# Kernel optimization log

Measured on AMD Instinct MI355X. Metric: run time of the kernel, lower is better.

## Reference

```python
import jax, jax.numpy as jnp
import numpy as np

B, Q, V, H = 8, 128, 512, 512


def setup_inputs() -> dict:
    key = jax.random.key(0)
    ks = jax.random.split(key, 6)
    s = 1.0 / np.sqrt(H)
    return {
        "query": jax.random.normal(ks[0], (B, Q, H), jnp.float32),
        "values": jax.random.normal(ks[1], (B, V, H), jnp.float32),
        "mask": jax.random.randint(ks[2], (B, V), 0, 2, jnp.int32),
        "Wq": jax.random.normal(ks[3], (H, H), jnp.float32) * s,
        "bq": jnp.zeros((H,), jnp.float32),
        "Wv": jax.random.normal(ks[4], (H, H), jnp.float32) * s,
        "bv": jnp.zeros((H,), jnp.float32),
        "wc": jax.random.normal(ks[5], (H, 1), jnp.float32) * s,
        "bc": jnp.zeros((1,), jnp.float32),
    }


def reference(query, values, mask, Wq, bq, Wv, bv, wc, bc):
    # Project once per token (Q*H and V*H GEMMs), then broadcast-add:
    # faithful to tanh(Lq(q)[:, :, None] + Lv(v)[:, None]) since Linear is
    # applied along the last dim and broadcasting commutes with it.
    qp = jnp.einsum('bqh,kh->bqk', query, Wq) + bq          # [B,Q,H]
    vp = jnp.einsum('bvh,kh->bvk', values, Wv) + bv          # [B,V,H]
    added = jnp.tanh(qp[:, :, None, :] + vp[:, None, :, :])  # [B,Q,V,H]
    scores = jnp.einsum('bqvh,ho->bqv', added, wc) + bc[0]   # [B,Q,V]
    neg_inf = jnp.array(-jnp.inf, scores.dtype)
    scores = jnp.where(mask[:, None, :] == 0, neg_inf, scores)
    weights = jax.nn.softmax(scores, axis=-1)                # [B,Q,V]
    context = jnp.einsum('bqv,bvh->bqh', weights, values)    # [B,Q,H]
    return (context, weights)
```

## Files before the change

kernel.cpp:

```cpp
#include <hip/hip_runtime.h>
#include <hip/hip_bf16.h>


#define C_SCALE 2.8853900817779268f

typedef __attribute__((ext_vector_type(8))) short short8;
typedef __attribute__((ext_vector_type(4))) float f32x4;

__device__ __forceinline__ float fexp2(float x) { return __builtin_amdgcn_exp2f(x); }
__device__ __forceinline__ float frcp(float x)  { return __builtin_amdgcn_rcpf(x); }
__device__ __forceinline__ short f2bf(float x) {
  __hip_bfloat16 h = __float2bfloat16(x);
  return __builtin_bit_cast(short, h);
}
__device__ __forceinline__ float bf2f(short s) {
  return __bfloat162float(__builtin_bit_cast(__hip_bfloat16, s));
}

__global__ __launch_bounds__(256) void proj_gemm_mfma(
    const float* __restrict__ query, const float* __restrict__ values,
    const float* __restrict__ Wq, const float* __restrict__ Wv,
    const float* __restrict__ bq, const float* __restrict__ bv,
    float* __restrict__ qp, float* __restrict__ vp)
{
  __shared__ short sAhi[64 * 72];
  __shared__ short sAlo[64 * 72];
  __shared__ short sWhi[64 * 72];
  __shared__ short sWlo[64 * 72];

  const int t    = threadIdx.x;
  const int lane = t & 63;
  const int w    = t >> 6;
  const int by   = blockIdx.y;
  const bool isQ = (by < 16);
  const float* A    = isQ ? query : values;
  const float* W    = isQ ? Wq : Wv;
  const float* bias = isQ ? bq : bv;
  float*       out  = isQ ? qp : vp;
  const int m0 = (isQ ? by : (by - 16)) << 6;
  const int n0 = blockIdx.x << 6;

  const int srow = t >> 2, scol = t & 3;
  const float* Ap = A + (size_t)(m0 + srow) * 512 + (scol << 2);
  const float* Wp = W + (size_t)(n0 + srow) * 512 + (scol << 2);

  const int mw = (w & 1) << 5, nw = (w >> 1) << 5;
  const int frow = lane & 15, fquad = lane >> 4;

  f32x4 acc[2][2] = {};
  float4 pfA[4], pfW[4];
#pragma unroll
  for (int p = 0; p < 4; ++p) {
    pfA[p] = *(const float4*)(Ap + (p << 4));
    pfW[p] = *(const float4*)(Wp + (p << 4));
  }

  for (int kc = 0; kc < 512; kc += 64) {
    __syncthreads();
#pragma unroll
    for (int p = 0; p < 4; ++p) {
      float av[4] = {pfA[p].x, pfA[p].y, pfA[p].z, pfA[p].w};
      float wv[4] = {pfW[p].x, pfW[p].y, pfW[p].z, pfW[p].w};
      short4 ah, al, wh, wl;
      short* ahp = (short*)&ah; short* alp = (short*)&al;
      short* whp = (short*)&wh; short* wlp = (short*)&wl;
#pragma unroll
      for (int k = 0; k < 4; ++k) {
        short h1 = f2bf(av[k]); ahp[k] = h1; alp[k] = f2bf(av[k] - bf2f(h1));
        short h2 = f2bf(wv[k]); whp[k] = h2; wlp[k] = f2bf(wv[k] - bf2f(h2));
      }
      const int ofs = srow * 72 + ((p << 2) + scol) * 4;
      *(short4*)&sAhi[ofs] = ah; *(short4*)&sAlo[ofs] = al;
      *(short4*)&sWhi[ofs] = wh; *(short4*)&sWlo[ofs] = wl;
    }
    __syncthreads();
    if (kc + 64 < 512) {
#pragma unroll
      for (int p = 0; p < 4; ++p) {
        pfA[p] = *(const float4*)(Ap + kc + 64 + (p << 4));
        pfW[p] = *(const float4*)(Wp + kc + 64 + (p << 4));
      }
    }
#pragma unroll
    for (int kb = 0; kb < 2; ++kb) {
      const int ko = kb * 32 + fquad * 8;
      short8 ahi[2], alo[2], whi[2], wlo[2];
#pragma unroll
      for (int mt = 0; mt < 2; ++mt) {
        const int r = (mw + mt * 16 + frow) * 72 + ko;
        ahi[mt] = *(const short8*)&sAhi[r];
        alo[mt] = *(const short8*)&sAlo[r];
      }
#pragma unroll
      for (int nt = 0; nt < 2; ++nt) {
        const int r = (nw + nt * 16 + frow) * 72 + ko;
        whi[nt] = *(const short8*)&sWhi[r];
        wlo[nt] = *(const short8*)&sWlo[r];
      }
#pragma unroll
      for (int mt = 0; mt < 2; ++mt)
#pragma unroll
        for (int nt = 0; nt < 2; ++nt) {
          acc[mt][nt] = __builtin_amdgcn_mfma_f32_16x16x32_bf16(
              alo[mt], whi[nt], acc[mt][nt], 0, 0, 0);
          acc[mt][nt] = __builtin_amdgcn_mfma_f32_16x16x32_bf16(
              ahi[mt], wlo[nt], acc[mt][nt], 0, 0, 0);
          acc[mt][nt] = __builtin_amdgcn_mfma_f32_16x16x32_bf16(
              ahi[mt], whi[nt], acc[mt][nt], 0, 0, 0);
        }
    }
  }

#pragma unroll
  for (int nt = 0; nt < 2; ++nt) {
    const int n = n0 + nw + nt * 16 + frow;
    const float bn = bias[n];
#pragma unroll
    for (int mt = 0; mt < 2; ++mt) {
      float vreg[4] = {acc[mt][nt].x, acc[mt][nt].y, acc[mt][nt].z, acc[mt][nt].w};
#pragma unroll
      for (int r = 0; r < 4; ++r) {
        const int m = m0 + mw + mt * 16 + fquad * 4 + r;
        out[(size_t)m * 512 + n] = vreg[r] + bn;
      }
    }
  }
}

__global__ __launch_bounds__(512) void attn_fused(
    const float* __restrict__ qp, const float* __restrict__ vp,
    const float* __restrict__ values, const int* __restrict__ mask,
    const float* __restrict__ wc,
    float* __restrict__ out_ctx, float* __restrict__ out_w)
{
  __shared__ int   idxs[512];
  __shared__ float wls[2][512];
  __shared__ float wls2[512][2];
  __shared__ int   cnt8[8];

  const int t    = threadIdx.x;
  const int lane = t & 63;
  const int w    = t >> 6;
  const int b    = blockIdx.x & 7;
  const int qg   = blockIdx.x >> 3;
  const int rowbase = b * 128 + qg * 2;

  ((float*)wls)[t]        = 3.4e38f;
  ((float*)wls)[t + 512]  = 3.4e38f;
  ((float*)wls2)[t]       = 0.f;
  ((float*)wls2)[t + 512] = 0.f;
  idxs[t] = 0;
  if (t < 256) {
    float4 z = {0.f, 0.f, 0.f, 0.f};
    ((float4*)(out_w + (size_t)rowbase * 512))[t] = z;
  }
  const int mv = mask[b * 512 + t];
  const unsigned long long bal = __ballot(mv != 0);
  if (lane == 0) cnt8[w] = __popcll(bal);
  __syncthreads();
  int cnt = 0, offw = 0;
#pragma unroll
  for (int j = 0; j < 8; ++j) { if (j == w) offw = cnt; cnt += cnt8[j]; }
  if (mv) {
    int rank = __popcll(bal & ((1ull << lane) - 1ull));
    idxs[offw + rank] = t;
  }
  __syncthreads();

  const int NSTEP = (cnt + 31) >> 5;
  const int sbase = w * (NSTEP << 2);
  const int g  = lane >> 4;
  const int c4 = (lane & 15) << 2;

  int   rows[16];
  float a0[16], a1[16];
#pragma unroll
  for (int i = 0; i < 16; ++i) {
    if (i >= NSTEP) break;
    rows[i] = idxs[sbase + (i << 2) + g];
    a0[i] = 0.f; a1[i] = 0.f;
  }

  const float* vpb = vp + (size_t)b * 512 * 512;
  const float* qr0 = qp + (size_t)rowbase * 512;
  const float* qr1 = qr0 + 512;

  for (int j = 0; j < 8; ++j) {
    const int hoff = j * 64 + c4;
    float4 q0v = *(const float4*)(qr0 + hoff);
    float4 q1v = *(const float4*)(qr1 + hoff);
    float4 wcv = *(const float4*)(wc + hoff);
    float cq0[4] = {C_SCALE * q0v.x, C_SCALE * q0v.y, C_SCALE * q0v.z, C_SCALE * q0v.w};
    float cq1[4] = {C_SCALE * q1v.x, C_SCALE * q1v.y, C_SCALE * q1v.z, C_SCALE * q1v.w};
    float wc4[4] = {wcv.x, wcv.y, wcv.z, wcv.w};

    float4 vcur = *(const float4*)(vpb + (size_t)rows[0] * 512 + hoff);
#pragma unroll
    for (int i = 0; i < 16; ++i) {
      if (i >= NSTEP) break;
      float4 vnext = vcur;
      if (i + 1 < NSTEP)
        vnext = *(const float4*)(vpb + (size_t)rows[i + 1] * 512 + hoff);
      float vv[4] = {vcur.x, vcur.y, vcur.z, vcur.w};
#pragma unroll
      for (int k = 0; k < 4; ++k) {
        float x0 = __builtin_fmaf(C_SCALE, vv[k], cq0[k]);
        float r0 = frcp(fexp2(x0) + 1.0f);
        a0[i] = __builtin_fmaf(wc4[k], r0, a0[i]);
        float x1 = __builtin_fmaf(C_SCALE, vv[k], cq1[k]);
        float r1 = frcp(fexp2(x1) + 1.0f);
        a1[i] = __builtin_fmaf(wc4[k], r1, a1[i]);
      }
      vcur = vnext;
    }
  }

#pragma unroll
  for (int i = 0; i < 16; ++i) {
    if (i >= NSTEP) break;
    float s0 = a0[i], s1 = a1[i];
#pragma unroll
    for (int off = 1; off < 16; off <<= 1) {
      s0 += __shfl_xor(s0, off, 64);
      s1 += __shfl_xor(s1, off, 64);
    }
    const int s = sbase + (i << 2) + g;
    if ((lane & 15) == i && s < cnt) { wls[0][s] = s0; wls[1][s] = s1; }
  }
  __syncthreads();

  {
    const int mq = (w >= 4) ? 1 : 0;
    const float* sc = wls[mq];
    float4 u0 = ((const float4*)sc)[lane * 2];
    float4 u1 = ((const float4*)sc)[lane * 2 + 1];
    float s8[8] = {u0.x, u0.y, u0.z, u0.w, u1.x, u1.y, u1.z, u1.w};
    float m = s8[0];
#pragma unroll
    for (int k = 1; k < 8; ++k) m = fminf(m, s8[k]);
#pragma unroll
    for (int off = 1; off < 64; off <<= 1) m = fminf(m, __shfl_xor(m, off, 64));
    float e[8], S = 0.f;
#pragma unroll
    for (int k = 0; k < 8; ++k) { e[k] = fexp2(C_SCALE * (m - s8[k])); S += e[k]; }
#pragma unroll
    for (int off = 1; off < 64; off <<= 1) S += __shfl_xor(S, off, 64);
    const float rinv = frcp(S);
    if (w == 0 || w == 4) {
      float* owq = out_w + (size_t)(rowbase + mq) * 512;
#pragma unroll
      for (int k = 0; k < 8; ++k) {
        const int s = lane * 8 + k;
        const float wgt = e[k] * rinv;
        wls2[s][mq] = wgt;
        if (s < cnt) owq[idxs[s]] = wgt;
      }
    }
  }
  __syncthreads();

  const int NC = (cnt + 3) >> 2;
  const int hbase = w * 64 + c4;
  const float* vb = values + (size_t)b * 512 * 512;
  float c0[4] = {0.f, 0.f, 0.f, 0.f}, c1[4] = {0.f, 0.f, 0.f, 0.f};
#pragma unroll 4
  for (int i = 0; i < NC; ++i) {
    const int s = (i << 2) + g;
    const int row = idxs[s];
    const float2 wg = *(const float2*)&wls2[s][0];
    const float4 v4 = *(const float4*)(vb + (size_t)row * 512 + hbase);
    float vv[4] = {v4.x, v4.y, v4.z, v4.w};
#pragma unroll
    for (int k = 0; k < 4; ++k) {
      c0[k] = __builtin_fmaf(wg.x, vv[k], c0[k]);
      c1[k] = __builtin_fmaf(wg.y, vv[k], c1[k]);
    }
  }
#pragma unroll
  for (int k = 0; k < 4; ++k) {
    c0[k] += __shfl_xor(c0[k], 16, 64); c0[k] += __shfl_xor(c0[k], 32, 64);
    c1[k] += __shfl_xor(c1[k], 16, 64); c1[k] += __shfl_xor(c1[k], 32, 64);
  }
  if (lane < 16) {
    float4 o0 = {c0[0], c0[1], c0[2], c0[3]};
    float4 o1 = {c1[0], c1[1], c1[2], c1[3]};
    *(float4*)(out_ctx + (size_t)rowbase * 512 + w * 64 + lane * 4)       = o0;
    *(float4*)(out_ctx + (size_t)(rowbase + 1) * 512 + w * 64 + lane * 4) = o1;
  }
}

extern "C" void kernel_launch(void* const* d_in, const int* in_sizes, int n_in,
                              void* d_out, int out_size, void* d_ws, size_t ws_size,
                              hipStream_t stream) {
  const float* query  = (const float*)d_in[0];
  const float* values = (const float*)d_in[1];
  const int*   mask   = (const int*)d_in[2];
  const float* Wq     = (const float*)d_in[3];
  const float* bq     = (const float*)d_in[4];
  const float* Wv     = (const float*)d_in[5];
  const float* bv     = (const float*)d_in[6];
  const float* wc     = (const float*)d_in[7];

  float* out = (float*)d_out;
  float* qp  = (float*)d_ws;
  float* vp  = qp + (size_t)1024 * 512;

  proj_gemm_mfma<<<dim3(8, 80), 256, 0, stream>>>(query, values, Wq, Wv, bq, bv, qp, vp);
  attn_fused<<<512, 512, 0, stream>>>(qp, vp, values, mask, wc,
                                      out, out + (size_t)8 * 128 * 512);
}
```

Before: 151.7 us.

## Share one exp2 across two query rows and simplify bf16 split and addressing

In the attention kernel, the second query row's exponential is obtained by multiplying the first row's exp2 result by a precomputed per-column factor exp2(C*(q1-q0)). This cuts the transcendental count in the hot loop from four to three per element. It risks overflow or precision loss when the q difference is large. The change also replaces the bf16 hi/lo split with integer rounding, switches gather offsets to 32-bit unsigned, and adds min-blocks launch bounds to both kernels, which may limit register allocation.

```diff
diff --git a/kernel.cpp b/kernel.cpp
--- a/kernel.cpp
+++ b/kernel.cpp
@@ -9,15 +9,19 @@
 
 __device__ __forceinline__ float fexp2(float x) { return __builtin_amdgcn_exp2f(x); }
 __device__ __forceinline__ float frcp(float x)  { return __builtin_amdgcn_rcpf(x); }
-__device__ __forceinline__ short f2bf(float x) {
-  __hip_bfloat16 h = __float2bfloat16(x);
-  return __builtin_bit_cast(short, h);
+
+__device__ __forceinline__ void bf_split(float x, short& hi, short& lo) {
+  unsigned u = __builtin_bit_cast(unsigned, x);
+  unsigned r = u + 0x7fffu + ((u >> 16) & 1u);
+  hi = (short)(r >> 16);
+  float hf = __builtin_bit_cast(float, r & 0xffff0000u);
+  float lf = x - hf;
+  unsigned ul = __builtin_bit_cast(unsigned, lf);
+  unsigned rl = ul + 0x7fffu + ((ul >> 16) & 1u);
+  lo = (short)(rl >> 16);
 }
-__device__ __forceinline__ float bf2f(short s) {
-  return __bfloat162float(__builtin_bit_cast(__hip_bfloat16, s));
-}
-
-__global__ __launch_bounds__(256) void proj_gemm_mfma(
+
+__global__ __launch_bounds__(256, 4) void proj_gemm_mfma(
     const float* __restrict__ query, const float* __restrict__ values,
     const float* __restrict__ Wq, const float* __restrict__ Wv,
     const float* __restrict__ bq, const float* __restrict__ bv,
@@ -66,8 +70,8 @@
       short* whp = (short*)&wh; short* wlp = (short*)&wl;
 #pragma unroll
       for (int k = 0; k < 4; ++k) {
-        short h1 = f2bf(av[k]); ahp[k] = h1; alp[k] = f2bf(av[k] - bf2f(h1));
-        short h2 = f2bf(wv[k]); whp[k] = h2; wlp[k] = f2bf(wv[k] - bf2f(h2));
+        bf_split(av[k], ahp[k], alp[k]);
+        bf_split(wv[k], whp[k], wlp[k]);
       }
       const int ofs = srow * 72 + ((p << 2) + scol) * 4;
       *(short4*)&sAhi[ofs] = ah; *(short4*)&sAlo[ofs] = al;
@@ -127,7 +131,7 @@
   }
 }
 
-__global__ __launch_bounds__(512) void attn_fused(
+__global__ __launch_bounds__(512, 4) void attn_fused(
     const float* __restrict__ qp, const float* __restrict__ vp,
     const float* __restrict__ values, const int* __restrict__ mask,
     const float* __restrict__ wc,
@@ -172,12 +176,12 @@
   const int g  = lane >> 4;
   const int c4 = (lane & 15) << 2;
 
-  int   rows[16];
+  unsigned voff[16];
   float a0[16], a1[16];
 #pragma unroll
   for (int i = 0; i < 16; ++i) {
     if (i >= NSTEP) break;
-    rows[i] = idxs[sbase + (i << 2) + g];
+    voff[i] = ((unsigned)idxs[sbase + (i << 2) + g] << 9) + (unsigned)c4;
     a0[i] = 0.f; a1[i] = 0.f;
   }
 
@@ -191,24 +195,27 @@
     float4 q1v = *(const float4*)(qr1 + hoff);
     float4 wcv = *(const float4*)(wc + hoff);
     float cq0[4] = {C_SCALE * q0v.x, C_SCALE * q0v.y, C_SCALE * q0v.z, C_SCALE * q0v.w};
-    float cq1[4] = {C_SCALE * q1v.x, C_SCALE * q1v.y, C_SCALE * q1v.z, C_SCALE * q1v.w};
+    float dd[4]  = {fexp2(C_SCALE * (q1v.x - q0v.x)), fexp2(C_SCALE * (q1v.y - q0v.y)),
+                    fexp2(C_SCALE * (q1v.z - q0v.z)), fexp2(C_SCALE * (q1v.w - q0v.w))};
     float wc4[4] = {wcv.x, wcv.y, wcv.z, wcv.w};
-
-    float4 vcur = *(const float4*)(vpb + (size_t)rows[0] * 512 + hoff);
+    const unsigned jo = (unsigned)(j * 64);
+
+    float4 vcur = *(const float4*)(vpb + (voff[0] + jo));
 #pragma unroll
     for (int i = 0; i < 16; ++i) {
       if (i >= NSTEP) break;
       float4 vnext = vcur;
       if (i + 1 < NSTEP)
-        vnext = *(const float4*)(vpb + (size_t)rows[i + 1] * 512 + hoff);
+        vnext = *(const float4*)(vpb + (voff[i + 1] + jo));
       float vv[4] = {vcur.x, vcur.y, vcur.z, vcur.w};
 #pragma unroll
       for (int k = 0; k < 4; ++k) {
         float x0 = __builtin_fmaf(C_SCALE, vv[k], cq0[k]);
-        float r0 = frcp(fexp2(x0) + 1.0f);
+        float e0 = fexp2(x0);
+        float e1 = e0 * dd[k];
+        float r0 = frcp(e0 + 1.0f);
+        float r1 = frcp(e1 + 1.0f);
         a0[i] = __builtin_fmaf(wc4[k], r0, a0[i]);
-        float x1 = __builtin_fmaf(C_SCALE, vv[k], cq1[k]);
-        float r1 = frcp(fexp2(x1) + 1.0f);
         a1[i] = __builtin_fmaf(wc4[k], r1, a1[i]);
       }
       vcur = vnext;
@@ -260,15 +267,15 @@
   __syncthreads();
 
   const int NC = (cnt + 3) >> 2;
-  const int hbase = w * 64 + c4;
+  const unsigned hbase = (unsigned)(w * 64 + c4);
   const float* vb = values + (size_t)b * 512 * 512;
   float c0[4] = {0.f, 0.f, 0.f, 0.f}, c1[4] = {0.f, 0.f, 0.f, 0.f};
 #pragma unroll 4
   for (int i = 0; i < NC; ++i) {
     const int s = (i << 2) + g;
-    const int row = idxs[s];
+    const unsigned ro = ((unsigned)idxs[s] << 9) + hbase;
     const float2 wg = *(const float2*)&wls2[s][0];
-    const float4 v4 = *(const float4*)(vb + (size_t)row * 512 + hbase);
+    const float4 v4 = *(const float4*)(vb + ro);
     float vv[4] = {v4.x, v4.y, v4.z, v4.w};
 #pragma unroll
     for (int k = 0; k < 4; ++k) {
```

Measured after the change: 149.0 us. Within noise of the previous version (-1.8%).
